# Kernel tuning notes

Hardware: AMD Instinct MI355X
Metric: run time of the kernel (lower is better)

Reference implementation:

```python
import jax, jax.numpy as jnp
import numpy as np

B, N, C_IN, C_EMB, G = 16, 1024, 16, 64, 128
NEG = -1e12


def _lap(m):
    # m @ D^-1/2, transpose, @ D^-1/2  (matches torch code incl. transpose)
    d = jnp.sum(m, axis=1) ** -0.5
    return (m * d[None, :]).T * d[None, :]


def setup_inputs():
    key = jax.random.key(0)
    ks = jax.random.split(key, 16)
    f = jax.random.normal
    return {
        'x': f(ks[0], (B, C_IN, N), jnp.float32),
        'ct': f(ks[1], (B, C_EMB, N), jnp.float32),
        'graph_data': jax.random.uniform(ks[2], (2, N, N), dtype=jnp.float32),
        'emb_w': f(ks[3], (C_EMB, C_IN)) / np.sqrt(C_IN).astype(np.float32),
        'emb_b': f(ks[4], (C_EMB,)) * 0.01,
        'emb2_w': f(ks[5], (N, N)) / np.sqrt(N).astype(np.float32),
        'emb2_b': f(ks[6], (N,)) * 0.01,
        'att_W': f(ks[7], (C_EMB, C_EMB)) / np.sqrt(C_EMB).astype(np.float32),
        'att_a': f(ks[8], (2 * C_EMB, 1)) / np.sqrt(2 * C_EMB).astype(np.float32),
        'att_GL': f(ks[9], (N, G)) / np.sqrt(G).astype(np.float32),
        'uai_w': f(ks[10], (C_EMB, C_EMB)) / np.sqrt(C_EMB).astype(np.float32),
        'uai_b': f(ks[11], (C_EMB,)) * 0.01,
        'lin1_w': f(ks[12], (C_EMB, C_EMB)) / np.sqrt(C_EMB).astype(np.float32),
        'lin2_w': f(ks[13], (C_EMB, C_EMB)) / np.sqrt(C_EMB).astype(np.float32),
        'lin2_b': f(ks[14], (C_EMB,)) * 0.01,
        'ln_w': jnp.ones((C_EMB, N), jnp.float32),
        'ln_b': jnp.zeros((C_EMB, N), jnp.float32),
    }


def reference(x, ct, graph_data, emb_w, emb_b, emb2_w, emb2_b, att_W, att_a,
              att_GL, uai_w, uai_b, lin1_w, lin2_w, lin2_b, ln_w, ln_b):
    # emb: Conv1d k=1 -> leaky_relu -> Linear over node axis N
    h0 = jax.nn.leaky_relu(jnp.einsum('bcn,ec->ben', x, emb_w) + emb_b[None, :, None])
    h0 = jnp.einsum('ben,mn->bem', h0, emb2_w) + emb2_b[None, None, :]
    inp = jnp.swapaxes(h0, 1, 2)  # [B,N,C']

    # InterpositionAttention (repeat/cat factorized: e_ij = leakyrelu(a1.h_i + a2.h_j))
    eye = jnp.eye(N, dtype=x.dtype)
    adj_att = jax.nn.softmax(jax.nn.relu(att_GL @ att_GL.T), axis=-1) + eye
    h = inp @ att_W  # [B,N,C']
    e = jax.nn.leaky_relu((h @ att_a[:C_EMB]) + jnp.swapaxes(h @ att_a[C_EMB:], 1, 2))  # [B,N,N]
    att = jax.nn.softmax(jnp.where(adj_att > 0, e, NEG), axis=2)
    x_att = jnp.swapaxes(jax.nn.relu(att @ h), 1, 2)  # [B,C',N]

    # UAI module (eval mode: dropout off -> all MC samples equal -> sigma = 0)
    mu = jnp.swapaxes(x_att, 1, 2) @ uai_w.T + uai_b  # [B,N,C']
    x_uai = jnp.swapaxes(mu, 1, 2)  # [B,C',N]

    g1 = _lap(graph_data[0] + eye)
    g2 = _lap(graph_data[1] + eye)

    # learned adjacency from pairwise squared distances (cdist p=2, squared)
    xf = jnp.swapaxes(x_uai, 1, 2)  # [B,N,C']
    sq = jnp.sum(xf * xf, axis=-1)
    d2 = jnp.maximum(sq[:, :, None] + sq[:, None, :] - 2.0 * (xf @ jnp.swapaxes(xf, 1, 2)), 0.0)
    gl = jax.nn.softmax(jnp.exp(-d2 / (2.0 * C_EMB)) + eye, axis=-1)  # sigma^2 = emb_size

    def ln(z):  # LayerNorm over last two dims [C', N]
        m = jnp.mean(z, axis=(1, 2), keepdims=True)
        v = jnp.var(z, axis=(1, 2), keepdims=True)
        return (z - m) / jnp.sqrt(v + 1e-5) * ln_w + ln_b

    l1 = lambda z: jnp.einsum('oc,bcn->bon', lin1_w, z)
    l2 = lambda z: jnp.einsum('oc,bcn->bon', lin2_w, z) + lin2_b[None, :, None]

    x_new = ln(l1(x_uai) @ gl + l1(l1(x_uai) @ g1) @ g2)
    ft = jax.nn.gelu(ln(l2(x_uai) @ gl + l2(l2(x_uai) @ g1) @ g2), approximate=False)
    rt = ft  # rt is computed by the identical expression (dropout off)

    ct_new = ft * ct + x_new - ft * x_new
    ht = rt * jax.nn.elu(ct_new) + x_uai - rt * x_uai
    return (ht, ct_new)
```

## Files before the change

### kernel.cpp

```cpp
#include <hip/hip_runtime.h>
#include <math.h>

typedef unsigned short u16;
typedef __attribute__((ext_vector_type(8))) short short8;
typedef __attribute__((ext_vector_type(4))) float floatx4;

constexpr int BATCH = 16;
constexpr int NI = 1024;
constexpr int CE = 64;
constexpr int CI = 16;
constexpr long long NN2  = (long long)NI * NI;
constexpr long long BCN  = (long long)BATCH * CE * NI;
constexpr long long BNv  = (long long)BATCH * NI;
constexpr long long BNN  = (long long)BATCH * NI * NI;
constexpr long long S1 = (long long)CE * NI;
constexpr long long S2 = 2 * S1;
constexpr int ZERON = (int)(2 * BNv + 80);

__device__ __forceinline__ float lrelu01(float x) { return x > 0.f ? x : 0.01f * x; }

__device__ __forceinline__ u16 f2bf(float f) {
  unsigned u = __builtin_bit_cast(unsigned, f);
  return (u16)((u + 0x7fffu + ((u >> 16) & 1u)) >> 16);
}
__device__ __forceinline__ float bf2f(u16 h) {
  unsigned u = ((unsigned)h) << 16;
  return __builtin_bit_cast(float, u);
}
__device__ __forceinline__ unsigned fkey(float f) {
  unsigned u = __builtin_bit_cast(unsigned, f);
  return (u & 0x80000000u) ? ~u : (u | 0x80000000u);
}
__device__ __forceinline__ float funkey(unsigned k) {
  unsigned u = (k & 0x80000000u) ? (k & 0x7fffffffu) : ~k;
  return __builtin_bit_cast(float, u);
}

__device__ __forceinline__ void gload16(const u16* g, u16* l) {
  __builtin_amdgcn_global_load_lds(
      (const __attribute__((address_space(1))) void*)g,
      (__attribute__((address_space(3))) void*)l, 16, 0, 0);
}

__device__ __forceinline__ void fence13() {
  __builtin_amdgcn_sched_barrier(0);
  asm volatile("s_waitcnt vmcnt(2) lgkmcnt(0)" ::: "memory");
  __builtin_amdgcn_s_barrier();
  __builtin_amdgcn_sched_barrier(0);
}

__device__ __forceinline__ void fence5() {
  __builtin_amdgcn_sched_barrier(0);
  asm volatile("s_waitcnt vmcnt(2) lgkmcnt(0)" ::: "memory");
  __builtin_amdgcn_s_barrier();
  __builtin_amdgcn_sched_barrier(0);
}

template<int N>
__device__ __forceinline__ void fence_bar() {
  __builtin_amdgcn_sched_barrier(0);
  if constexpr (N == 0) asm volatile("s_waitcnt vmcnt(0)" ::: "memory");
  else if constexpr (N == 1) asm volatile("s_waitcnt vmcnt(1)" ::: "memory");
  else if constexpr (N == 2) asm volatile("s_waitcnt vmcnt(2)" ::: "memory");
  else if constexpr (N == 3) asm volatile("s_waitcnt vmcnt(3)" ::: "memory");
  else if constexpr (N == 4) asm volatile("s_waitcnt vmcnt(4)" ::: "memory");
  else if constexpr (N == 6) asm volatile("s_waitcnt vmcnt(6)" ::: "memory");
  else asm volatile("s_waitcnt vmcnt(0)" ::: "memory");
  __builtin_amdgcn_s_barrier();
  __builtin_amdgcn_sched_barrier(0);
}

template<int BM, int BN, int MODE>
__global__ __launch_bounds__(256) void mgemm(
    const u16* __restrict__ Ag, const u16* __restrict__ B1g, const u16* __restrict__ B2g,
    int K1, int K, int lda, int ldb, long long bsA, long long bsB1,
    float* __restrict__ Cf, u16* __restrict__ Cb, int ldc, long long bsC,
    const float* __restrict__ aux1, const float* __restrict__ aux2,
    const float* __restrict__ aux3, const float* __restrict__ aux4,
    float* __restrict__ Zout)
{
  constexpr int RM = BM / 2, RN = BN / 2, MI = RM / 16, NJ = RN / 16;
  constexpr bool PIPE3 = (MODE == 14 || MODE == 15);
  constexpr int NBB = PIPE3 ? 3 : (MODE == 13 ? 3 : (MODE == 5 ? 2 : 1));
  constexpr int NBA = PIPE3 ? 3 : (MODE == 13 ? 2 : (MODE == 5 ? 3 : 1));
  constexpr int NLA = (BM * 8) / 256;
  constexpr int NLB = (BN * 8) / 256;
  constexpr int L = (NLA + NLB);
  __shared__ __align__(16) u16 As[NBA * BM * 64];
  __shared__ __align__(16) u16 Bs[NBB * BN * 64];
  __shared__ __align__(16) u16 xa[MODE == 13 ? 32 * 72 : 1];
  const int tid = threadIdx.x;
  int z, n0, r0, job15 = 0;
  bool job4 = false;
  long long cboff = 0;
  if constexpr (MODE == 15) {
    const int id = blockIdx.x;
    if (id >= 512 && id < 1536) {
      const int m = id - 512;
      float s = 0.f, sv = 0.f;
      for (int n = tid; n < NI; n += 256) {
        float g = aux3[(long long)m * NI + n] * aux2[n];
        s += g;
        sv = fmaf(g, aux1[n], sv);
      }
      float* r1 = (float*)As;
      float* r2 = (float*)As + 256;
      r1[tid] = s; r2[tid] = sv; __syncthreads();
      for (int st = 128; st > 0; st >>= 1) {
        if (tid < st) { r1[tid] += r1[tid + st]; r2[tid] += r2[tid + st]; }
        __syncthreads();
      }
      if (tid == 0) {
        float dm = aux2[m];
        Cf[m] = dm * (r1[0] + dm);
        Zout[m] = dm * (r2[0] + dm * aux1[m]);
      }
      return;
    }
    if (id >= 1536) {
      const int id2 = id - 1536;
      job15 = 2;
      z = id2 >> 5; r0 = (id2 & 1) * BM; n0 = ((id2 >> 1) & 15) * BN;
    } else {
      z = 0; n0 = (id & 15) * BN; r0 = (id >> 4) * BM;
    }
  } else if constexpr (MODE == 5) {
    const int fid = blockIdx.x;
    const int xcd = fid & 7, idx = fid >> 3;
    const int code = (idx >> 5) * 8 + xcd;
    z = code >> 1; r0 = (code & 1) * BM; n0 = (idx & 31) * BN;
  } else if constexpr (MODE == 3) {
    const int id = blockIdx.x;
    if (id < 4096) {
      const int xcd = id & 7, idx = id >> 3;
      z = (idx >> 8) * 8 + xcd;
      const int g = idx & 255;
      n0 = (g & 15) * 64; r0 = ((g >> 4) & 15) * 64;
    } else {
      const int t4 = id - 4096;
      job4 = true;
      z = t4 >> 6;
      const int g = t4 & 63;
      r0 = (g >> 4) * 64;
      n0 = (g & 15) * 64;
    }
  } else if constexpr (MODE == 13 || MODE == 14) {
    const int id = blockIdx.x;
    const int xcd = id & 7, idx = id >> 3;
    z = (idx >> 5) * 8 + xcd;
    if constexpr (MODE == 13) { r0 = (idx & 31) * BM; n0 = 0; }
    else { n0 = (idx & 31) * BN; r0 = 0; }
  } else {
    z = blockIdx.z; n0 = blockIdx.x * BN; r0 = blockIdx.y * BM;
  }
  int Kv = K, K1v = K1, ldav = lda, ldbv = ldb;
  const u16 *Ab, *Bb1;
  if constexpr (MODE == 15) {
    if (job15 == 2) {
      Kv = 64; K1v = 128; ldav = 64; ldbv = 64;
      Ab = B2g + (long long)r0 * 64;
      Bb1 = (const u16*)aux4 + (long long)z * S1 + (long long)n0 * 64;
      cboff = bsB1 + (long long)z * S1;
    } else {
      Ab = Ag + (long long)r0 * lda;
      Bb1 = B1g + (long long)n0 * ldb;
    }
  } else {
    Ab = Ag + (long long)z * bsA + (long long)r0 * ldav;
    Bb1 = B1g + (long long)z * bsB1 + (long long)n0 * ldbv;
    if constexpr (MODE == 3) {
      if (job4) Ab = ((const u16*)aux2) + (long long)r0 * 64;
    }
  }
  const int lane = tid & 63;
  const int wid = tid >> 6;
  const int wr = wid >> 1, wc = wid & 1;
  const int q = lane >> 4, mlow = lane & 15;
  const int wbase = tid & ~63;

  floatx4 acc[MI][NJ] = {};
  float zp0 = 0.f;

  float s1r_13 = 0.f, mr_13 = 0.f;
  const float* s2z_13 = nullptr;
  float4 sa, sb;
  if constexpr (MODE == 13) {
    const float* s1z = aux2 + (long long)z * NI;
    s2z_13 = aux3 + (long long)z * NI;
    const float mb = funkey(((const unsigned*)aux4)[z]);
    s1r_13 = s1z[r0 + (tid >> 3)];
    mr_13 = lrelu01(s1r_13 + mb);
  }

  auto stageAB = [&](int buf, int k0) {
    if constexpr (MODE != 13) {
      const u16* Asrc = Ab + k0;
#pragma unroll
      for (int s = 0; s < NLA; s++) {
        int cid = tid + s * 256;
        int r = cid >> 3, cc = cid & 7;
        gload16(Asrc + (long long)r * ldav + ((cc ^ (r & 7)) << 3),
                As + buf * (BM * 64) + ((wbase + s * 256) << 3));
      }
    }
    const u16* Bsrc = (k0 < K1v) ? (Bb1 + k0)
                                 : (B2g + (long long)n0 * ldbv + (k0 - K1v));
#pragma unroll
    for (int s = 0; s < NLB; s++) {
      int cid = tid + s * 256;
      int r = cid >> 3, cc = cid & 7;
      gload16(Bsrc + (long long)r * ldbv + ((cc ^ (r & 7)) << 3),
              Bs + buf * (BN * 64) + ((wbase + s * 256) << 3));
    }
  };

  auto agen_ld = [&](int k0) {
    const float* sp = s2z_13 + k0 + (tid & 7) * 8;
    sa = *(const float4*)sp;
    sb = *(const float4*)(sp + 4);
  };
  auto agen_st = [&](int buf) {
    int r = tid >> 3, craw = tid & 7;
    float p0 = __expf(lrelu01(s1r_13 + sa.x) - mr_13);
    float p1 = __expf(lrelu01(s1r_13 + sa.y) - mr_13);
    float p2 = __expf(lrelu01(s1r_13 + sa.z) - mr_13);
    float p3 = __expf(lrelu01(s1r_13 + sa.w) - mr_13);
    float p4 = __expf(lrelu01(s1r_13 + sb.x) - mr_13);
    float p5 = __expf(lrelu01(s1r_13 + sb.y) - mr_13);
    float p6 = __expf(lrelu01(s1r_13 + sb.z) - mr_13);
    float p7 = __expf(lrelu01(s1r_13 + sb.w) - mr_13);
    zp0 += p0 + p1 + p2 + p3 + p4 + p5 + p6 + p7;
    uint4 v;
    v.x = (unsigned)f2bf(p0) | ((unsigned)f2bf(p1) << 16);
    v.y = (unsigned)f2bf(p2) | ((unsigned)f2bf(p3) << 16);
    v.z = (unsigned)f2bf(p4) | ((unsigned)f2bf(p5) << 16);
    v.w = (unsigned)f2bf(p6) | ((unsigned)f2bf(p7) << 16);
    *(uint4*)&As[buf * (BM * 64) + (r * 8 + (craw ^ (r & 7))) * 8] = v;
  };

  auto compute_tile = [&](int bufA, int bufB) {
#pragma unroll
    for (int kh = 0; kh < 2; kh++) {
      const int kc = kh * 4 + q;
      short8 afr[MI], bfr[NJ];
#pragma unroll
      for (int i = 0; i < MI; i++) {
        int row = wr * RM + i * 16 + mlow;
        afr[i] = *(const short8*)&As[bufA * (BM * 64) + (row * 8 + (kc ^ (row & 7))) * 8];
      }
#pragma unroll
      for (int j = 0; j < NJ; j++) {
        int row = wc * RN + j * 16 + mlow;
        bfr[j] = *(const short8*)&Bs[bufB * (BN * 64) + (row * 8 + (kc ^ (row & 7))) * 8];
      }
#pragma unroll
      for (int i = 0; i < MI; i++)
#pragma unroll
        for (int j = 0; j < NJ; j++)
          acc[i][j] = __builtin_amdgcn_mfma_f32_16x16x32_bf16(afr[i], bfr[j], acc[i][j], 0, 0, 0);
    }
  };

  if constexpr (PIPE3) {
    const int nk = Kv >> 6;
#pragma unroll
    for (int p = 0; p < 2; p++) {
      int kk = (p < nk) ? p : (nk - 1);
      stageAB(p, kk << 6);
    }
    fence_bar<L>();
    int cur = 0, stg = 2;
    for (int ki = 0; ki < nk; ki++) {
      if (ki + 2 < nk) stageAB(stg, (ki + 2) << 6);
      compute_tile(cur, cur);
      if (ki + 1 < nk) {
        const int rem = nk - 1 - ki;
        const int u = (rem < 2) ? rem : 2;
        if (u == 2) fence_bar<L>();
        else fence_bar<0>();
      }
      cur++; if (cur == NBB) cur = 0;
      stg++; if (stg == NBB) stg = 0;
    }
    __syncthreads();
  } else if constexpr (MODE == 5) {
    const int nk = Kv >> 6;
    const float* Zg = Cf + (long long)z * NI;
    uint4 bv; float4 bz0, bz1;
    const int br = tid >> 3, bcc = tid & 7;
    auto aglo = [&](int kt, int buf) {
      const u16* Asrc = Ab + (kt << 6);
#pragma unroll
      for (int s = 0; s < NLA; s++) {
        int cid = tid + s * 256;
        int r = cid >> 3, cc = cid & 7;
        gload16(Asrc + (long long)r * ldav + ((cc ^ (r & 7)) << 3),
                As + buf * (BM * 64) + ((wbase + s * 256) << 3));
      }
    };
    auto bld = [&](int kt) {
      const int k0 = kt << 6;
      const u16* Bsrc = (k0 < K1v) ? (Bb1 + k0)
                                   : (B2g + (long long)n0 * ldbv + (k0 - K1v));
      bv = *(const uint4*)(Bsrc + (long long)br * ldbv + bcc * 8);
      if (k0 < K1v) {
        bz0 = *(const float4*)(Zg + k0 + bcc * 8);
        bz1 = *(const float4*)(Zg + k0 + bcc * 8 + 4);
      }
    };
    auto bst = [&](int kt, int buf) {
      uint4 w = bv;
      if ((kt << 6) < K1v) {
        float f0 = bf2f((u16)(w.x & 0xffff)) * __builtin_amdgcn_rcpf(bz0.x);
        float f1 = bf2f((u16)(w.x >> 16))    * __builtin_amdgcn_rcpf(bz0.y);
        float f2 = bf2f((u16)(w.y & 0xffff)) * __builtin_amdgcn_rcpf(bz0.z);
        float f3 = bf2f((u16)(w.y >> 16))    * __builtin_amdgcn_rcpf(bz0.w);
        float f4 = bf2f((u16)(w.z & 0xffff)) * __builtin_amdgcn_rcpf(bz1.x);
        float f5 = bf2f((u16)(w.z >> 16))    * __builtin_amdgcn_rcpf(bz1.y);
        float f6 = bf2f((u16)(w.w & 0xffff)) * __builtin_amdgcn_rcpf(bz1.z);
        float f7 = bf2f((u16)(w.w >> 16))    * __builtin_amdgcn_rcpf(bz1.w);
        w.x = (unsigned)f2bf(f0) | ((unsigned)f2bf(f1) << 16);
        w.y = (unsigned)f2bf(f2) | ((unsigned)f2bf(f3) << 16);
        w.z = (unsigned)f2bf(f4) | ((unsigned)f2bf(f5) << 16);
        w.w = (unsigned)f2bf(f6) | ((unsigned)f2bf(f7) << 16);
      }
      *(uint4*)&Bs[buf * (BN * 64) + (br * 8 + (bcc ^ (br & 7))) * 8] = w;
    };
    bld(0); aglo(0, 0); aglo(1, 1); bst(0, 0);
    fence5();
    for (int ki = 0; ki < nk; ki++) {
      if (ki + 1 < nk) bld(ki + 1);
      if (ki + 2 < nk) aglo(ki + 2, (ki + 2) % 3);
      if (ki + 1 < nk) bst(ki + 1, (ki + 1) & 1);
      compute_tile(ki % 3, ki & 1);
      fence5();
    }
    __syncthreads();
  } else if constexpr (MODE == 13) {
    const int nk = Kv >> 6;
    agen_ld(0);
    stageAB(0, 0);
    if (nk > 1) stageAB(1, 64);
    agen_st(0);
    fence13();
    for (int ki = 0; ki < nk; ki++) {
      if (ki + 1 < nk) agen_ld((ki + 1) << 6);
      if (ki + 2 < nk) stageAB((ki + 2) % 3, (ki + 2) << 6);
      if (ki + 1 < nk) agen_st((ki + 1) & 1);
      compute_tile(ki & 1, ki % 3);
      fence13();
    }
  } else {
    for (int k0 = 0; k0 < Kv; k0 += 64) {
      stageAB(0, k0);
      __syncthreads();
      compute_tile(0, 0);
      __syncthreads();
    }
  }

  if constexpr (MODE == 3) {
    if (job4) {
      u16* abig = (u16*)Cf;
#pragma unroll
      for (int i = 0; i < MI; i++) {
#pragma unroll
        for (int j = 0; j < NJ; j++) {
#pragma unroll
          for (int rg = 0; rg < 4; rg++) {
            int r = r0 + wr * RM + i * 16 + q * 4 + rg;
            int ncol = n0 + wc * RN + j * 16 + mlow;
            int blk = r >> 6, oo = r & 63;
            int drow = ((blk & 1) << 6) + oo;
            float v = acc[i][j][rg];
            if (blk < 2) v += aux3[drow];
            abig[(long long)z * (128 * 2048LL) + (long long)drow * 2048 +
                 (long long)(blk >> 1) * 1024 + ncol] = f2bf(v);
          }
        }
      }
    } else {
      const float* sqb = aux1 + (long long)z * NI;
#pragma unroll
      for (int i = 0; i < MI; i++) {
#pragma unroll
        for (int rg = 0; rg < 4; rg++) {
          int r = r0 + wr * RM + i * 16 + q * 4 + rg;
          float sqi = sqb[r];
          float rsum = 0.f;
#pragma unroll
          for (int j = 0; j < NJ; j++) {
            int ncol = n0 + wc * RN + j * 16 + mlow;
            float d2 = fmaxf(sqi + sqb[ncol] - 2.f * acc[i][j][rg], 0.f);
            float w = __expf(__expf(-d2 * (1.f / 128.f)) + (r == ncol ? 1.f : 0.f) - 2.f);
            Cb[(long long)z * bsC + (long long)r * ldc + ncol] = f2bf(w);
            rsum += w;
          }
          rsum += __shfl_xor(rsum, 1);
          rsum += __shfl_xor(rsum, 2);
          rsum += __shfl_xor(rsum, 4);
          rsum += __shfl_xor(rsum, 8);
          if (mlow == 0) atomicAdd(&Zout[(long long)z * NI + r], rsum);
        }
      }
    }
  } else if constexpr (MODE == 14) {
    float ps1 = 0.f, ps2 = 0.f;
#pragma unroll
    for (int i = 0; i < MI; i++) {
#pragma unroll
      for (int rg = 0; rg < 4; rg++) {
        int r = wr * RM + i * 16 + q * 4 + rg;
        int ncol = n0 + wc * RN + mlow;
        float v = acc[i][0][rg] + aux3[r] * aux1[ncol];
        Cb[(long long)z * bsC + (long long)r * ldc + ncol] = f2bf(v);
        ps1 = fmaf(v, aux2[r], ps1);
        ps2 = fmaf(v, aux2[64 + r], ps2);
      }
    }
    ps1 += __shfl_xor(ps1, 16); ps1 += __shfl_xor(ps1, 32);
    ps2 += __shfl_xor(ps2, 16); ps2 += __shfl_xor(ps2, 32);
    float* sred = (float*)As;
    const int col = wc * RN + mlow;
    if (q == 0) { sred[col * 2 + wr] = ps1; sred[64 + col * 2 + wr] = ps2; }
    __syncthreads();
    if (tid < 32) {
      float v1 = sred[tid * 2] + sred[tid * 2 + 1];
      float v2 = sred[64 + tid * 2] + sred[64 + tid * 2 + 1];
      Cf[(long long)z * NI + n0 + tid] = v1;
      Zout[(long long)z * NI + n0 + tid] = v2;
      float mx = v2;
      for (int off = 1; off < 32; off <<= 1) mx = fmaxf(mx, __shfl_xor(mx, off));
      if (tid == 0) atomicMax((unsigned*)B2g + z, fkey(mx));
    }
  } else if constexpr (MODE == 13) {
    float* zred = (float*)xa;
    float* zinv = (float*)xa + 256;
    zred[(tid >> 3) * 8 + (tid & 7)] = zp0;
    __syncthreads();
    if (tid < 32) {
      float sum = 0.f;
#pragma unroll
      for (int j = 0; j < 8; j++) sum += zred[tid * 8 + j];
      zinv[tid] = 1.f / sum;
    }
    __syncthreads();
    float zr[4];
#pragma unroll
    for (int rg = 0; rg < 4; rg++) zr[rg] = zinv[wr * 16 + q * 4 + rg];
    __syncthreads();
#pragma unroll
    for (int j = 0; j < NJ; j++) {
#pragma unroll
      for (int rg = 0; rg < 4; rg++) {
        int row = wr * 16 + q * 4 + rg;
        int col = wc * RN + j * 16 + mlow;
        float v = fmaxf(acc[0][j][rg] * zr[rg], 0.f);
        xa[row * 72 + col] = f2bf(v);
      }
    }
#pragma unroll
    for (int s = 0; s < 2; s++) {
      int cid = tid + s * 256;
      int r = cid >> 3, cc = cid & 7;
      gload16(B2g + r * 64 + ((cc ^ (r & 7)) << 3),
              Bs + ((wbase + s * 256) << 3));
    }
    __syncthreads();
    floatx4 acc2[2] = {};
#pragma unroll
    for (int kh = 0; kh < 2; kh++) {
      const int kc = kh * 4 + q;
      short8 a2 = *(const short8*)&xa[(wr * 16 + mlow) * 72 + kc * 8];
#pragma unroll
      for (int j = 0; j < 2; j++) {
        int orow = wc * 32 + j * 16 + mlow;
        short8 b2 = *(const short8*)&Bs[(orow * 8 + (kc ^ (orow & 7))) * 8];
        acc2[j] = __builtin_amdgcn_mfma_f32_16x16x32_bf16(a2, b2, acc2[j], 0, 0, 0);
      }
    }
#pragma unroll
    for (int rg = 0; rg < 4; rg++) {
      int row = r0 + wr * 16 + q * 4 + rg;
      float sqp = 0.f;
#pragma unroll
      for (int j = 0; j < 2; j++) {
        int o = wc * 32 + j * 16 + mlow;
        float v = acc2[j][rg] + aux1[o];
        Cb[(long long)z * bsC + (long long)row * ldc + o] = f2bf(v);
        sqp = fmaf(v, v, sqp);
      }
      sqp += __shfl_xor(sqp, 1);
      sqp += __shfl_xor(sqp, 2);
      sqp += __shfl_xor(sqp, 4);
      sqp += __shfl_xor(sqp, 8);
      if (mlow == 0) atomicAdd(&Zout[(long long)z * NI + row], sqp);
    }
  } else if constexpr (MODE == 5) {
    float ts = 0.f, tss = 0.f;
#pragma unroll
    for (int i = 0; i < MI; i++) {
#pragma unroll
      for (int j = 0; j < NJ; j++) {
#pragma unroll
        for (int rg = 0; rg < 4; rg++) {
          int r = r0 + wr * RM + i * 16 + q * 4 + rg;
          int ncol = n0 + wc * RN + j * 16 + mlow;
          float v = acc[i][j][rg];
          v += aux3[r] * aux1[ncol] + aux4[r] * aux2[ncol];
          Cb[(long long)z * bsC + (long long)r * ldc + ncol] = f2bf(v);
          ts += v;
          tss = fmaf(v, v, tss);
        }
      }
    }
    float* red = (float*)As;
    red[tid] = ts; red[256 + tid] = tss;
    __syncthreads();
    for (int st = 128; st > 0; st >>= 1) {
      if (tid < st) { red[tid] += red[tid + st]; red[256 + tid] += red[256 + tid + st]; }
      __syncthreads();
    }
    if (tid == 0) {
      const int half = r0 >> 6;
      atomicAdd(&Zout[z * 2 + half], red[0]);
      atomicAdd(&Zout[32 + z * 2 + half], red[256]);
    }
  } else {
#pragma unroll
    for (int i = 0; i < MI; i++) {
#pragma unroll
      for (int j = 0; j < NJ; j++) {
#pragma unroll
        for (int rg = 0; rg < 4; rg++) {
          int r = r0 + wr * RM + i * 16 + q * 4 + rg;
          int ncol = n0 + wc * RN + j * 16 + mlow;
          Cb[cboff + (long long)r * ldc + ncol] = f2bf(acc[i][j][rg]);
        }
      }
    }
  }
}

__global__ __launch_bounds__(256) void lap_rowsum(const float* __restrict__ gd,
                                                  float* __restrict__ dr,
                                                  float* __restrict__ zero)
{
  if (blockIdx.x >= 2048) {
    int i = (blockIdx.x - 2048) * 256 + threadIdx.x;
    if (i < ZERON) zero[i] = 0.f;
    return;
  }
  const int ki = blockIdx.x;
  const float* row = gd + (long long)ki * NI;
  float s = 0.f;
  for (int j = threadIdx.x; j < NI; j += 256) s += row[j];
  __shared__ float red[256];
  red[threadIdx.x] = s; __syncthreads();
  for (int st = 128; st > 0; st >>= 1) {
    if (threadIdx.x < st) red[threadIdx.x] += red[threadIdx.x + st];
    __syncthreads();
  }
  if (threadIdx.x == 0) dr[ki] = rsqrtf(red[0] + 1.f);
}

__global__ __launch_bounds__(256) void mega_prep(
    const float* __restrict__ l1w, const float* __restrict__ l2w,
    const float* __restrict__ l2b, const float* __restrict__ uaiw,
    const float* __restrict__ attW,
    u16* __restrict__ stack4, float* __restrict__ rb2ext, float* __restrict__ rl2ext,
    u16* __restrict__ uaiw_bf, u16* __restrict__ attwT_bf, float* __restrict__ wcs,
    const float* __restrict__ emb2w, u16* __restrict__ emb2w_bf,
    const float* __restrict__ x, const float* __restrict__ ew,
    const float* __restrict__ eb, u16* __restrict__ h0aT,
    const float* __restrict__ gd, const float* __restrict__ dsum,
    u16* __restrict__ g2t, u16* __restrict__ g1,
    float* __restrict__ cs1)
{
  __shared__ float sm[1092];
  const int bid = blockIdx.x;
  const int t = threadIdx.x;
  if (bid < 98) {
    const int gid = bid * 256 + t;
    if (gid < 4096) {
      stack4[gid] = f2bf(l1w[gid]);
    } else if (gid < 8192) {
      stack4[gid] = f2bf(l2w[gid - 4096]);
    } else if (gid < 12288) {
      int tt = gid - 8192, o = tt >> 6, m = tt & 63;
      float s = 0.f;
      for (int c = 0; c < 64; c++) s = fmaf(l1w[o * 64 + c], l1w[c * 64 + m], s);
      stack4[gid] = f2bf(s);
    } else if (gid < 16384) {
      int tt = gid - 12288, o = tt >> 6, m = tt & 63;
      float s = 0.f;
      for (int c = 0; c < 64; c++) s = fmaf(l2w[o * 64 + c], l2w[c * 64 + m], s);
      stack4[gid] = f2bf(s);
    } else if (gid < 16512) {
      int r = gid - 16384;
      rb2ext[r] = (r < 64) ? 0.f : l2b[r - 64];
    } else if (gid < 16640) {
      int r = gid - 16512;
      float v = 0.f;
      if (r >= 64) { int o = r - 64; for (int c = 0; c < 64; c++) v = fmaf(l2w[o * 64 + c], l2b[c], v); }
      rl2ext[r] = v;
    } else if (gid < 20736) {
      uaiw_bf[gid - 16640] = f2bf(uaiw[gid - 16640]);
    } else if (gid < 24832) {
      int idx = gid - 20736;
      int c = idx >> 6, e = idx & 63;
      attwT_bf[idx] = f2bf(attW[e * 64 + c]);
    } else if (gid < 24896) {
      int c = gid - 24832;
      float s = 0.f;
      for (int e = 0; e < 64; e++) s += attW[e * 64 + c];
      wcs[c] = s;
    }
  } else if (bid < 1122) {
    const long long i = (long long)(bid - 98) * 1024 + t * 4;
    float4 v = *(const float4*)(emb2w + i);
    u16 o4[4] = {f2bf(v.x), f2bf(v.y), f2bf(v.z), f2bf(v.w)};
    *(uint2*)(emb2w_bf + i) = *(const uint2*)o4;
  } else if (bid < 1378) {
    const int sub = bid - 1122;
    const int b = sub >> 4;
    const int nc = (sub & 15) * 64;
    float* we = sm;
    float* be = sm + 1024;
    for (int i = t; i < 1024; i += 256) we[i] = ew[i];
    if (t < 64) be[t] = eb[t];
    __syncthreads();
    const int n = nc + (t >> 2);
    const int e0 = (t & 3) * 16;
    const float* xb = x + (long long)b * CI * NI + n;
    float xv[16];
#pragma unroll
    for (int c = 0; c < CI; c++) xv[c] = xb[(long long)c * NI];
    u16 out16[16];
#pragma unroll
    for (int ee = 0; ee < 16; ee++) {
      const int e = e0 + ee;
      float a = be[e];
#pragma unroll
      for (int c = 0; c < CI; c++) a = fmaf(xv[c], we[e * 16 + c], a);
      out16[ee] = f2bf(lrelu01(a));
    }
    u16* dst = h0aT + (long long)b * S1 + (long long)n * 64 + e0;
    *(uint4*)dst = *(uint4*)out16;
    *(uint4*)(dst + 8) = *(uint4*)(out16 + 8);
  } else if (bid < 2402) {
    const int m = bid - 1378;
    const int j = t * 4;
    const float* d = dsum + NI;
    float4 g = *(const float4*)(gd + NN2 + (long long)m * NI + j);
    float dm = d[m];
    float4 dj = *(const float4*)(d + j);
    u16 o4[4];
    o4[0] = f2bf((g.x + (m == j     ? 1.f : 0.f)) * dm * dj.x);
    o4[1] = f2bf((g.y + (m == j + 1 ? 1.f : 0.f)) * dm * dj.y);
    o4[2] = f2bf((g.z + (m == j + 2 ? 1.f : 0.f)) * dm * dj.z);
    o4[3] = f2bf((g.w + (m == j + 3 ? 1.f : 0.f)) * dm * dj.w);
    *(uint2*)(g2t + (long long)m * NI + j) = *(const uint2*)o4;
  } else if (bid < 3426) {
    const int sub = bid - 2402;
    const int bx = (sub & 31) * 32, by = (sub >> 5) * 32;
    const int lx = t & 31, ly = t >> 5;
    float* tile = sm;
    for (int yy = ly; yy < 32; yy += 8)
      tile[yy * 33 + lx] = gd[(long long)(by + yy) * NI + bx + lx];
    __syncthreads();
    for (int yy = ly; yy < 32; yy += 8) {
      const int i = bx + yy, j = by + lx;
      float v = (tile[lx * 33 + yy] + (i == j ? 1.f : 0.f)) * dsum[i] * dsum[j];
      g1[(long long)i * NI + j] = f2bf(v);
    }
  } else {
    const int n = bid - 3426;
    float s = 0.f;
    for (int i = t; i < NI; i += 256) s = fmaf(gd[(long long)n * NI + i], dsum[i], s);
    float* red = sm;
    red[t] = s; __syncthreads();
    for (int st = 128; st > 0; st >>= 1) {
      if (t < st) red[t] += red[t + st];
      __syncthreads();
    }
    if (t == 0) cs1[n] = dsum[n] * (red[0] + dsum[n]);
  }
}

__global__ __launch_bounds__(512) void ln_final_t(const u16* __restrict__ T,
                                                  const float* __restrict__ stats,
                                                  const float* __restrict__ lnw,
                                                  const float* __restrict__ lnb,
                                                  const float* __restrict__ ct,
                                                  const u16* __restrict__ xuT,
                                                  float* __restrict__ outp)
{
  __shared__ float xs[64 * 65];
  const int blk = blockIdx.x;
  const int b = blk >> 4;
  const int n0 = (blk & 15) << 6;
  const int t = threadIdx.x;
  const int tc = t & 63, tr = t >> 6;
#pragma unroll
  for (int i = 0; i < 8; i++) {
    int nn = i * 8 + tr;
    xs[tc * 65 + nn] = bf2f(xuT[((long long)b << 16) + (long long)(n0 + nn) * 64 + tc]);
  }
  __syncthreads();
  const float inv_n = 1.f / 65536.f;
  const float m0 = stats[b * 2] * inv_n;
  const float m1 = stats[b * 2 + 1] * inv_n;
  const float rs0 = rsqrtf(fmaxf(stats[32 + b * 2] * inv_n - m0 * m0, 0.f) + 1e-5f);
  const float rs1 = rsqrtf(fmaxf(stats[32 + b * 2 + 1] * inv_n - m1 * m1, 0.f) + 1e-5f);
#pragma unroll
  for (int j = 0; j < 8; j++) {
    const int c = j * 8 + tr;
    const int n = n0 + tc;
    const int rem = c * NI + n;
    const long long toff = (long long)b * S2 + rem;
    const float t0 = bf2f(T[toff]);
    const float t1 = bf2f(T[toff + S1]);
    const float w = lnw[rem], bb = lnb[rem];
    const float xn = (t0 - m0) * rs0 * w + bb;
    float ft = (t1 - m1) * rs1 * w + bb;
    ft = 0.5f * ft * (1.f + erff(ft * 0.70710678118654752f));
    const float u = xs[c * 65 + tc];
    const long long oidx = ((long long)b << 16) + rem;
    const float cn = fmaf(ft, ct[oidx] - xn, xn);
    const float el = cn > 0.f ? cn : expm1f(cn);
    outp[oidx] = fmaf(ft, el - u, u);
    outp[BCN + oidx] = cn;
  }
}

extern "C" void kernel_launch(void* const* d_in, const int* in_sizes, int n_in,
                              void* d_out, int out_size, void* d_ws, size_t ws_size,
                              hipStream_t stream)
{
  (void)in_sizes; (void)n_in; (void)out_size; (void)ws_size;
  const float* x      = (const float*)d_in[0];
  const float* ct     = (const float*)d_in[1];
  const float* gdata  = (const float*)d_in[2];
  const float* emb_w  = (const float*)d_in[3];
  const float* emb_b  = (const float*)d_in[4];
  const float* emb2_w = (const float*)d_in[5];
  const float* emb2_b = (const float*)d_in[6];
  const float* att_W  = (const float*)d_in[7];
  const float* att_a  = (const float*)d_in[8];
  const float* uai_w  = (const float*)d_in[10];
  const float* uai_b  = (const float*)d_in[11];
  const float* lin1_w = (const float*)d_in[12];
  const float* lin2_w = (const float*)d_in[13];
  const float* lin2_b = (const float*)d_in[14];
  const float* ln_w   = (const float*)d_in[15];
  const float* ln_b   = (const float*)d_in[16];
  float* outp = (float*)d_out;

  float* ws = (float*)d_ws;
  long long o = 0;
  auto af = [&](long long n) { float* p = ws + o; o += (n + 63) & ~63LL; return p; };
  auto au = [&](long long n) { return (u16*)af((n + 1) / 2); };

  float* s1      = af(BNv);
  float* s2      = af(BNv);
  float* dsum    = af(2 * NI);
  float* cs1v    = af(NI);
  float* cs2v    = af(NI);
  float* v2v     = af(NI);
  float* rb2ext  = af(128);
  float* rl2ext  = af(128);
  float* wcs     = af(64);
  float* zeroreg = af(ZERON);
  float* Zgl     = zeroreg;
  float* sqv     = zeroreg + BNv;
  float* stats   = zeroreg + 2 * BNv;
  unsigned* s2mU = (unsigned*)(stats + 64);
  u16* Tacc      = au(S2 * BATCH);
  u16* emb2w_bf  = au(NN2);
  u16* h0aTb     = au(S1 * BATCH);
  u16* ybf       = au(S1 * BATCH);
  u16* hTb       = au(S1 * BATCH);
  u16* xuaiTb    = au(S1 * BATCH);
  u16* g1b       = au(NN2);
  u16* g2tb      = au(NN2);
  u16* G12b      = au(NN2);
  u16* Abig      = au((long long)BATCH * 128 * 2048);
  u16* stack4    = au(256 * 64);
  u16* uaiw_bf   = au(CE * CE);
  u16* attwT_bf  = au(CE * CE);
  u16* bigW      = au(BNN);

  lap_rowsum<<<2048 + (ZERON + 255) / 256, 256, 0, stream>>>(gdata, dsum, zeroreg);

  mega_prep<<<4450, 256, 0, stream>>>(
      lin1_w, lin2_w, lin2_b, uai_w, att_W,
      stack4, rb2ext, rl2ext, uaiw_bf, attwT_bf, wcs,
      emb2_w, emb2w_bf, x, emb_w, emb_b, h0aTb,
      gdata, dsum, g2tb, g1b, cs1v);

  mgemm<32, 64, 15><<<2048, 256, 0, stream>>>(
      g2tb, g1b, attwT_bf, NI, NI, NI, NI, 0, (long long)(ybf - G12b),
      cs2v, G12b, NI, 0, cs1v, dsum + NI, gdata + NN2, (const float*)h0aTb, v2v);

  mgemm<64, 32, 14><<<512, 256, 0, stream>>>(
      ybf, emb2w_bf, (const u16*)s2mU, NI, NI, NI, NI, S1, 0,
      s1, hTb, NI, S1, emb2_b, att_a, wcs, nullptr, s2);

  mgemm<32, 64, 13><<<512, 256, 0, stream>>>(
      hTb, hTb, uaiw_bf, NI, NI, NI, NI, 0, S1,
      nullptr, xuaiTb, CE, S1, uai_b, s1, s2, (const float*)s2mU, sqv);

  mgemm<64, 64, 3><<<5120, 256, 0, stream>>>(
      xuaiTb, xuaiTb, nullptr, CE, CE, CE, CE, S1, S1,
      (float*)Abig, bigW, NI, NN2, sqv, (const float*)stack4, rb2ext, nullptr, Zgl);

  mgemm<64, 32, 5><<<1024, 256, 0, stream>>>(
      Abig, bigW, G12b, NI, 2 * NI, 2048, NI, (long long)128 * 2048, NN2,
      Zgl, Tacc, NI, S2, cs2v, v2v, rb2ext, rl2ext, stats);

  ln_final_t<<<256, 512, 0, stream>>>(Tacc, stats, ln_w, ln_b, ct, xuaiTb, outp);
}
```

Measured before the change: 222.7 us.

## Stage Z scale vector in LDS and double-buffer B register prefetch in MODE 5

In the MODE 5 GEMM, the per-column normalisation vector Z is now loaded once into shared memory with an async global-to-LDS load, instead of being reloaded from global memory on every K step. B-tile register loads are double-buffered two steps ahead, and the loop is unrolled by two so global latency has more time to hide. The wait count in fence5 is raised to match the extra outstanding loads. The cost is more registers and LDS, and the unrolled loop assumes an even number of K tiles (it calls bst for ki+1 unconditionally).

Result: no change. 221.7 us (-0.5%).

```diff
diff --git a/kernel.cpp b/kernel.cpp
--- a/kernel.cpp
+++ b/kernel.cpp
@@ -51,7 +51,7 @@
 
 __device__ __forceinline__ void fence5() {
   __builtin_amdgcn_sched_barrier(0);
-  asm volatile("s_waitcnt vmcnt(2) lgkmcnt(0)" ::: "memory");
+  asm volatile("s_waitcnt vmcnt(3) lgkmcnt(0)" ::: "memory");
   __builtin_amdgcn_s_barrier();
   __builtin_amdgcn_sched_barrier(0);
 }
@@ -89,6 +89,7 @@
   __shared__ __align__(16) u16 As[NBA * BM * 64];
   __shared__ __align__(16) u16 Bs[NBB * BN * 64];
   __shared__ __align__(16) u16 xa[MODE == 13 ? 32 * 72 : 1];
+  __shared__ __align__(16) float zbuf[MODE == 5 ? 1024 : 1];
   const int tid = threadIdx.x;
   int z, n0, r0, job15 = 0;
   bool job4 = false;
@@ -286,7 +287,7 @@
   } else if constexpr (MODE == 5) {
     const int nk = Kv >> 6;
     const float* Zg = Cf + (long long)z * NI;
-    uint4 bv; float4 bz0, bz1;
+    uint4 bv0, bv1;
     const int br = tid >> 3, bcc = tid & 7;
     auto aglo = [&](int kt, int buf) {
       const u16* Asrc = Ab + (kt << 6);
@@ -298,27 +299,23 @@
                 As + buf * (BM * 64) + ((wbase + s * 256) << 3));
       }
     };
-    auto bld = [&](int kt) {
+    auto bld = [&](int kt, uint4& dst) {
       const int k0 = kt << 6;
       const u16* Bsrc = (k0 < K1v) ? (Bb1 + k0)
                                    : (B2g + (long long)n0 * ldbv + (k0 - K1v));
-      bv = *(const uint4*)(Bsrc + (long long)br * ldbv + bcc * 8);
-      if (k0 < K1v) {
-        bz0 = *(const float4*)(Zg + k0 + bcc * 8);
-        bz1 = *(const float4*)(Zg + k0 + bcc * 8 + 4);
-      }
+      dst = *(const uint4*)(Bsrc + (long long)br * ldbv + bcc * 8);
     };
-    auto bst = [&](int kt, int buf) {
-      uint4 w = bv;
+    auto bst = [&](int kt, uint4 w, int buf) {
       if ((kt << 6) < K1v) {
-        float f0 = bf2f((u16)(w.x & 0xffff)) * __builtin_amdgcn_rcpf(bz0.x);
-        float f1 = bf2f((u16)(w.x >> 16))    * __builtin_amdgcn_rcpf(bz0.y);
-        float f2 = bf2f((u16)(w.y & 0xffff)) * __builtin_amdgcn_rcpf(bz0.z);
-        float f3 = bf2f((u16)(w.y >> 16))    * __builtin_amdgcn_rcpf(bz0.w);
-        float f4 = bf2f((u16)(w.z & 0xffff)) * __builtin_amdgcn_rcpf(bz1.x);
-        float f5 = bf2f((u16)(w.z >> 16))    * __builtin_amdgcn_rcpf(bz1.y);
-        float f6 = bf2f((u16)(w.w & 0xffff)) * __builtin_amdgcn_rcpf(bz1.z);
-        float f7 = bf2f((u16)(w.w >> 16))    * __builtin_amdgcn_rcpf(bz1.w);
+        const float* zp = zbuf + (kt << 6) + bcc * 8;
+        float f0 = bf2f((u16)(w.x & 0xffff)) * __builtin_amdgcn_rcpf(zp[0]);
+        float f1 = bf2f((u16)(w.x >> 16))    * __builtin_amdgcn_rcpf(zp[1]);
+        float f2 = bf2f((u16)(w.y & 0xffff)) * __builtin_amdgcn_rcpf(zp[2]);
+        float f3 = bf2f((u16)(w.y >> 16))    * __builtin_amdgcn_rcpf(zp[3]);
+        float f4 = bf2f((u16)(w.z & 0xffff)) * __builtin_amdgcn_rcpf(zp[4]);
+        float f5 = bf2f((u16)(w.z >> 16))    * __builtin_amdgcn_rcpf(zp[5]);
+        float f6 = bf2f((u16)(w.w & 0xffff)) * __builtin_amdgcn_rcpf(zp[6]);
+        float f7 = bf2f((u16)(w.w >> 16))    * __builtin_amdgcn_rcpf(zp[7]);
         w.x = (unsigned)f2bf(f0) | ((unsigned)f2bf(f1) << 16);
         w.y = (unsigned)f2bf(f2) | ((unsigned)f2bf(f3) << 16);
         w.z = (unsigned)f2bf(f4) | ((unsigned)f2bf(f5) << 16);
@@ -326,13 +323,26 @@
       }
       *(uint4*)&Bs[buf * (BN * 64) + (br * 8 + (bcc ^ (br & 7))) * 8] = w;
     };
-    bld(0); aglo(0, 0); aglo(1, 1); bst(0, 0);
-    fence5();
-    for (int ki = 0; ki < nk; ki++) {
-      if (ki + 1 < nk) bld(ki + 1);
+    gload16((const u16*)Zg + tid * 8, (u16*)zbuf + (wbase << 3));
+    bld(0, bv0); bld(1, bv1);
+    aglo(0, 0); aglo(1, 1);
+    fence_bar<2>();
+    bst(0, bv0, 0);
+    asm volatile("s_waitcnt lgkmcnt(0)" ::: "memory");
+    __builtin_amdgcn_sched_barrier(0);
+    __builtin_amdgcn_s_barrier();
+    __builtin_amdgcn_sched_barrier(0);
+    for (int ki = 0; ki < nk; ki += 2) {
+      if (ki + 2 < nk) bld(ki + 2, bv0);
       if (ki + 2 < nk) aglo(ki + 2, (ki + 2) % 3);
-      if (ki + 1 < nk) bst(ki + 1, (ki + 1) & 1);
+      bst(ki + 1, bv1, (ki + 1) & 1);
       compute_tile(ki % 3, ki & 1);
+      fence5();
+      const int kj = ki + 1;
+      if (kj + 2 < nk) bld(kj + 2, bv1);
+      if (kj + 2 < nk) aglo(kj + 2, (kj + 2) % 3);
+      if (kj + 1 < nk) bst(kj + 1, bv0, (kj + 1) & 1);
+      compute_tile(kj % 3, kj & 1);
       fence5();
     }
     __syncthreads();
```

## Move softmax-denominator scaling into separate kernel and stream B via async LDS loads

Applied to the files above, without the earlier changes.

The MODE 5 GEMM used to load B through registers, scale it by the reciprocal of the softmax normaliser Zgl, and store it to LDS. The new code divides the normaliser into the A buffer (Abig) in place with a new small kernel, adiv, before the GEMM runs. Both A and B can then be staged by direct global-to-LDS loads in 128-wide K stages with a three-buffer pipeline and a new compute routine. This removes register round trips and per-element rcp work from the GEMM main loop, at the cost of an extra launch and an extra read-modify-write pass over Abig. The scaling also moves from the B operand to Abig, so whether Zgl indexing matches what the old code did should be checked.

Measured after the change: 225.3 us. Within noise of the previous version (+1.2%).

```diff
diff --git a/kernel.cpp b/kernel.cpp
--- a/kernel.cpp
+++ b/kernel.cpp
@@ -43,13 +43,6 @@
 }
 
 __device__ __forceinline__ void fence13() {
-  __builtin_amdgcn_sched_barrier(0);
-  asm volatile("s_waitcnt vmcnt(2) lgkmcnt(0)" ::: "memory");
-  __builtin_amdgcn_s_barrier();
-  __builtin_amdgcn_sched_barrier(0);
-}
-
-__device__ __forceinline__ void fence5() {
   __builtin_amdgcn_sched_barrier(0);
   asm volatile("s_waitcnt vmcnt(2) lgkmcnt(0)" ::: "memory");
   __builtin_amdgcn_s_barrier();
@@ -81,13 +74,15 @@
 {
   constexpr int RM = BM / 2, RN = BN / 2, MI = RM / 16, NJ = RN / 16;
   constexpr bool PIPE3 = (MODE == 14 || MODE == 15);
-  constexpr int NBB = PIPE3 ? 3 : (MODE == 13 ? 3 : (MODE == 5 ? 2 : 1));
-  constexpr int NBA = PIPE3 ? 3 : (MODE == 13 ? 2 : (MODE == 5 ? 3 : 1));
+  constexpr int NBB = PIPE3 ? 3 : (MODE == 13 ? 3 : 1);
+  constexpr int NBA = PIPE3 ? 3 : (MODE == 13 ? 2 : 1);
   constexpr int NLA = (BM * 8) / 256;
   constexpr int NLB = (BN * 8) / 256;
   constexpr int L = (NLA + NLB);
-  __shared__ __align__(16) u16 As[NBA * BM * 64];
-  __shared__ __align__(16) u16 Bs[NBB * BN * 64];
+  constexpr int ASZ = (MODE == 5) ? 3 * BM * 128 : NBA * BM * 64;
+  constexpr int BSZ = (MODE == 5) ? 3 * BN * 128 : NBB * BN * 64;
+  __shared__ __align__(16) u16 As[ASZ];
+  __shared__ __align__(16) u16 Bs[BSZ];
   __shared__ __align__(16) u16 xa[MODE == 13 ? 32 * 72 : 1];
   const int tid = threadIdx.x;
   int z, n0, r0, job15 = 0;
@@ -127,8 +122,10 @@
   } else if constexpr (MODE == 5) {
     const int fid = blockIdx.x;
     const int xcd = fid & 7, idx = fid >> 3;
-    const int code = (idx >> 5) * 8 + xcd;
-    z = code >> 1; r0 = (code & 1) * BM; n0 = (idx & 31) * BN;
+    const int idx2 = idx >> 5;
+    z = xcd + (idx2 >> 1) * 8;
+    r0 = (idx2 & 1) * BM;
+    n0 = (idx & 31) * BN;
   } else if constexpr (MODE == 3) {
     const int id = blockIdx.x;
     if (id < 4096) {
@@ -284,56 +281,68 @@
     }
     __syncthreads();
   } else if constexpr (MODE == 5) {
-    const int nk = Kv >> 6;
-    const float* Zg = Cf + (long long)z * NI;
-    uint4 bv; float4 bz0, bz1;
-    const int br = tid >> 3, bcc = tid & 7;
-    auto aglo = [&](int kt, int buf) {
-      const u16* Asrc = Ab + (kt << 6);
-#pragma unroll
-      for (int s = 0; s < NLA; s++) {
-        int cid = tid + s * 256;
-        int r = cid >> 3, cc = cid & 7;
-        gload16(Asrc + (long long)r * ldav + ((cc ^ (r & 7)) << 3),
-                As + buf * (BM * 64) + ((wbase + s * 256) << 3));
+    const int ns = Kv >> 7;
+    auto stage5 = [&](int buf, int s) {
+#pragma unroll
+      for (int sub = 0; sub < 2; sub++) {
+        const int k0 = (s << 7) + (sub << 6);
+        const u16* Asrc = Ab + k0;
+#pragma unroll
+        for (int g = 0; g < NLA; g++) {
+          int cid = tid + g * 256;
+          int r = cid >> 3, cc = cid & 7;
+          gload16(Asrc + (long long)r * ldav + ((cc ^ (r & 7)) << 3),
+                  As + buf * (BM * 128) + sub * (BM * 64) + ((wbase + g * 256) << 3));
+        }
+        const u16* Bsrc = (k0 < K1v) ? (Bb1 + k0)
+                                     : (B2g + (long long)n0 * ldbv + (k0 - K1v));
+#pragma unroll
+        for (int g = 0; g < NLB; g++) {
+          int cid = tid + g * 256;
+          int r = cid >> 3, cc = cid & 7;
+          gload16(Bsrc + (long long)r * ldbv + ((cc ^ (r & 7)) << 3),
+                  Bs + buf * (BN * 128) + sub * (BN * 64) + ((wbase + g * 256) << 3));
+        }
       }
     };
-    auto bld = [&](int kt) {
-      const int k0 = kt << 6;
-      const u16* Bsrc = (k0 < K1v) ? (Bb1 + k0)
-                                   : (B2g + (long long)n0 * ldbv + (k0 - K1v));
-      bv = *(const uint4*)(Bsrc + (long long)br * ldbv + bcc * 8);
-      if (k0 < K1v) {
-        bz0 = *(const float4*)(Zg + k0 + bcc * 8);
-        bz1 = *(const float4*)(Zg + k0 + bcc * 8 + 4);
+    auto compute5 = [&](int buf) {
+#pragma unroll
+      for (int sub = 0; sub < 2; sub++) {
+#pragma unroll
+        for (int kh = 0; kh < 2; kh++) {
+          const int kc = kh * 4 + q;
+          short8 afr[MI], bfr[NJ];
+#pragma unroll
+          for (int i = 0; i < MI; i++) {
+            int row = wr * RM + i * 16 + mlow;
+            afr[i] = *(const short8*)&As[buf * (BM * 128) + sub * (BM * 64) +
+                                         (row * 8 + (kc ^ (row & 7))) * 8];
+          }
+#pragma unroll
+          for (int j = 0; j < NJ; j++) {
+            int row = wc * RN + j * 16 + mlow;
+            bfr[j] = *(const short8*)&Bs[buf * (BN * 128) + sub * (BN * 64) +
+                                         (row * 8 + (kc ^ (row & 7))) * 8];
+          }
+#pragma unroll
+          for (int i = 0; i < MI; i++)
+#pragma unroll
+            for (int j = 0; j < NJ; j++)
+              acc[i][j] = __builtin_amdgcn_mfma_f32_16x16x32_bf16(afr[i], bfr[j], acc[i][j], 0, 0, 0);
+        }
       }
     };
-    auto bst = [&](int kt, int buf) {
-      uint4 w = bv;
-      if ((kt << 6) < K1v) {
-        float f0 = bf2f((u16)(w.x & 0xffff)) * __builtin_amdgcn_rcpf(bz0.x);
-        float f1 = bf2f((u16)(w.x >> 16))    * __builtin_amdgcn_rcpf(bz0.y);
-        float f2 = bf2f((u16)(w.y & 0xffff)) * __builtin_amdgcn_rcpf(bz0.z);
-        float f3 = bf2f((u16)(w.y >> 16))    * __builtin_amdgcn_rcpf(bz0.w);
-        float f4 = bf2f((u16)(w.z & 0xffff)) * __builtin_amdgcn_rcpf(bz1.x);
-        float f5 = bf2f((u16)(w.z >> 16))    * __builtin_amdgcn_rcpf(bz1.y);
-        float f6 = bf2f((u16)(w.w & 0xffff)) * __builtin_amdgcn_rcpf(bz1.z);
-        float f7 = bf2f((u16)(w.w >> 16))    * __builtin_amdgcn_rcpf(bz1.w);
-        w.x = (unsigned)f2bf(f0) | ((unsigned)f2bf(f1) << 16);
-        w.y = (unsigned)f2bf(f2) | ((unsigned)f2bf(f3) << 16);
-        w.z = (unsigned)f2bf(f4) | ((unsigned)f2bf(f5) << 16);
-        w.w = (unsigned)f2bf(f6) | ((unsigned)f2bf(f7) << 16);
-      }
-      *(uint4*)&Bs[buf * (BN * 64) + (br * 8 + (bcc ^ (br & 7))) * 8] = w;
-    };
-    bld(0); aglo(0, 0); aglo(1, 1); bst(0, 0);
-    fence5();
-    for (int ki = 0; ki < nk; ki++) {
-      if (ki + 1 < nk) bld(ki + 1);
-      if (ki + 2 < nk) aglo(ki + 2, (ki + 2) % 3);
-      if (ki + 1 < nk) bst(ki + 1, (ki + 1) & 1);
-      compute_tile(ki % 3, ki & 1);
-      fence5();
+    stage5(0, 0);
+    stage5(1, 1);
+    fence_bar<6>();
+    for (int ki = 0; ki < ns; ki++) {
+      if (ki + 2 < ns) stage5((ki + 2) % 3, ki + 2);
+      compute5(ki % 3);
+      if (ki + 1 < ns) {
+        const int rem = ns - 1 - ki;
+        if (rem >= 2) fence_bar<6>();
+        else fence_bar<0>();
+      }
     }
     __syncthreads();
   } else if constexpr (MODE == 13) {
@@ -539,6 +548,33 @@
         }
       }
     }
+  }
+}
+
+__global__ __launch_bounds__(256) void adiv(u16* __restrict__ abig,
+                                            const float* __restrict__ Zgl)
+{
+  const int bid = blockIdx.x;
+  const int z = bid >> 6;
+  const int r = (bid & 63) * 2;
+  const int t = threadIdx.x;
+  const int c = t * 4;
+  const float4 zv = *(const float4*)(Zgl + (long long)z * NI + c);
+  const float i0 = __builtin_amdgcn_rcpf(zv.x);
+  const float i1 = __builtin_amdgcn_rcpf(zv.y);
+  const float i2 = __builtin_amdgcn_rcpf(zv.z);
+  const float i3 = __builtin_amdgcn_rcpf(zv.w);
+  u16* base = abig + (long long)z * (128 * 2048LL) + (long long)r * 2048 + c;
+#pragma unroll
+  for (int rr = 0; rr < 2; rr++) {
+    u16* p = base + (long long)rr * 2048;
+    uint2 v = *(uint2*)p;
+    u16 o[4];
+    o[0] = f2bf(bf2f((u16)(v.x & 0xffff)) * i0);
+    o[1] = f2bf(bf2f((u16)(v.x >> 16)) * i1);
+    o[2] = f2bf(bf2f((u16)(v.y & 0xffff)) * i2);
+    o[3] = f2bf(bf2f((u16)(v.y >> 16)) * i3);
+    *(uint2*)p = *(uint2*)o;
   }
 }
 
@@ -815,9 +851,11 @@
       xuaiTb, xuaiTb, nullptr, CE, CE, CE, CE, S1, S1,
       (float*)Abig, bigW, NI, NN2, sqv, (const float*)stack4, rb2ext, nullptr, Zgl);
 
+  adiv<<<1024, 256, 0, stream>>>(Abig, Zgl);
+
   mgemm<64, 32, 5><<<1024, 256, 0, stream>>>(
       Abig, bigW, G12b, NI, 2 * NI, 2048, NI, (long long)128 * 2048, NN2,
-      Zgl, Tacc, NI, S2, cs2v, v2v, rb2ext, rl2ext, stats);
+      nullptr, Tacc, NI, S2, cs2v, v2v, rb2ext, rl2ext, stats);
 
   ln_final_t<<<256, 512, 0, stream>>>(Tacc, stats, ln_w, ln_b, ct, xuaiTb, outp);
 }
```
